# Optimization experiments

Measured on AMD Instinct MI355X. Metric: run time of the kernel, lower is better.

## Reference

```python
import jax, jax.numpy as jnp
import numpy as np

B, T, D = 2, 1024, 1024
H = 8            # num_heads
DK = 128         # head_k_dim
DV = 128         # head_v_dim
M = 128          # num_slots (== head_k_dim by default)
K = 32           # topk
EPS = 1e-5
SCALE = 1.0


def _rmsnorm(x, w, eps=EPS):
    return x * jax.lax.rsqrt(jnp.mean(x * x, axis=-1, keepdims=True) + eps) * w


def setup_inputs() -> dict:
    key = jax.random.key(0)
    ks = jax.random.split(key, 12)
    def lin(k, fan_in, fan_out):
        return jax.random.normal(k, (fan_in, fan_out), jnp.float32) / np.sqrt(fan_in).astype(np.float32)
    hidden_states = jax.random.normal(ks[0], (B, T, D), jnp.float32)
    Wq = lin(ks[1], D, H * DK)
    Wk = lin(ks[2], D, H * DK)
    Wv = lin(ks[3], D, H * DV)
    Wr = lin(ks[4], D, H * M)
    Wa = lin(ks[5], D, H)
    # Mamba2-style decay params
    A_log = jnp.log(jax.random.uniform(ks[6], (H,), jnp.float32, 1e-3, 16.0))
    dt = jnp.exp(jax.random.uniform(ks[7], (H,), jnp.float32) * (np.log(0.1) - np.log(0.001)) + np.log(0.001))
    dt = jnp.clip(dt, 1e-4, None)
    dt_bias = dt + jnp.log(-jnp.expm1(-dt))
    q_norm_w = jnp.ones((DK,), jnp.float32) + 0.01 * jax.random.normal(ks[8], (DK,), jnp.float32)
    k_norm_w = jnp.ones((DK,), jnp.float32) + 0.01 * jax.random.normal(ks[9], (DK,), jnp.float32)
    g_norm_w = jnp.ones((D,), jnp.float32) + 0.01 * jax.random.normal(ks[10], (D,), jnp.float32)
    Wo = lin(ks[11], H * DV, D)
    return dict(hidden_states=hidden_states, Wq=Wq, Wk=Wk, Wv=Wv, Wr=Wr, Wa=Wa,
                A_log=A_log, dt_bias=dt_bias, q_norm_w=q_norm_w, k_norm_w=k_norm_w,
                g_norm_w=g_norm_w, Wo=Wo)


def reference(hidden_states, Wq, Wk, Wv, Wr, Wa, A_log, dt_bias, q_norm_w, k_norm_w, g_norm_w, Wo):
    b, t, d = hidden_states.shape
    # projections
    q = (hidden_states @ Wq).reshape(b, t, H, DK)
    k = (hidden_states @ Wk).reshape(b, t, H, DK)
    v = jax.nn.silu((hidden_states @ Wv).reshape(b, t, H, DV))
    router = (hidden_states @ Wr).reshape(b, t, H, M)
    # Mamba2 decay (log-space, per head)
    f_head = -jnp.exp(A_log) * jax.nn.softplus(hidden_states @ Wa + dt_bias)  # [b,t,H]
    # swish feature map + per-head RMSNorm
    q = _rmsnorm(jax.nn.silu(q), q_norm_w)
    k = _rmsnorm(jax.nn.silu(k), k_norm_w)
    # sigmoid router scores, top-k slot routing (eval: no gumbel noise)
    scores = jax.nn.sigmoid(router)                    # [b,t,H,M]
    top_w, top_i = jax.lax.top_k(scores, K)            # [b,t,H,K]
    top_w = top_w / (jnp.sum(top_w, axis=-1, keepdims=True) + 1e-9)
    n = b * t * H
    rows = jnp.arange(n)[:, None]
    s_multihot = jnp.zeros((n, M), scores.dtype).at[rows, top_i.reshape(n, K)].set(
        top_w.reshape(n, K)).reshape(b, t, H, M)
    f = f_head[..., None] * s_multihot                 # [b,t,H,M], log decay per slot
    s = 1.0 - jnp.exp(f)                               # write gate per slot
    # decayed linear-attention recurrence over slots (M == DK):
    #   S_t[i,j] = exp(f_t[i]) * S_{t-1}[i,j] + s_t[i]*k_t[i]*v_t[j]
    #   o_t[j]   = scale * sum_i q_t[i] * S_t[i,j]
    def step(S, xs):
        q_t, k_t, v_t, f_t, s_t = xs                   # [b,H,*]
        S = jnp.exp(f_t)[..., None] * S + (s_t * k_t)[..., None] * v_t[..., None, :]
        o_t = jnp.einsum('bhk,bhkv->bhv', q_t, S) * SCALE
        return S, o_t
    xs = tuple(jnp.swapaxes(a, 0, 1) for a in (q, k, v, f, s))  # time-major
    S0 = jnp.zeros((b, H, DK, DV), q.dtype)
    _, o = jax.lax.scan(step, S0, xs)                  # o: [t,b,H,DV]
    o = jnp.swapaxes(o, 0, 1).reshape(b, t, H * DV)
    o = _rmsnorm(o, g_norm_w)                          # g_norm over hidden_size
    return o @ Wo
```

## Files before the change

### kernel.cpp

```cpp
#include <hip/hip_runtime.h>
#include <stdint.h>
#include <stddef.h>

#define H_ 8
#define T_ 1024

typedef __attribute__((ext_vector_type(8))) short s16x8;
typedef __attribute__((ext_vector_type(4))) float f32x4;
typedef __attribute__((ext_vector_type(16))) float f32x16;

static __device__ __forceinline__ unsigned short f2bf(float f){
  unsigned u = __float_as_uint(f);
  u += 0x7fffu + ((u >> 16) & 1u);
  return (unsigned short)(u >> 16);
}
static __device__ __forceinline__ float bf2f(unsigned short b){
  return __uint_as_float(((unsigned)b) << 16);
}
static __device__ __forceinline__ unsigned int pack_hl(float x){
  unsigned short h = f2bf(x);
  unsigned short l = f2bf(x - bf2f(h));
  return ((unsigned int)h << 16) | l;
}
static __device__ __forceinline__ void gl_lds16(const unsigned short* g, unsigned short* l){
  __builtin_amdgcn_global_load_lds((const __attribute__((address_space(1))) unsigned int*)g,
                                   (__attribute__((address_space(3))) unsigned int*)l,
                                   16, 0, 0);
}

__global__ void prep_k(const float* __restrict__ X, const float* __restrict__ Wa,
                       const float* __restrict__ A_log, const float* __restrict__ dtb,
                       unsigned short* __restrict__ hi, unsigned short* __restrict__ lo,
                       float* __restrict__ fh){
  __shared__ float xs[1024];
  int n = blockIdx.x, tid = threadIdx.x;
  size_t base = (size_t)n*1024 + tid*4;
  float4 x = *(const float4*)&X[base];
  *(float4*)&xs[tid*4] = x;
  float v[4] = {x.x,x.y,x.z,x.w};
  ushort4 h4, l4;
  unsigned short hh[4], ll[4];
#pragma unroll
  for(int j=0;j<4;j++){ hh[j]=f2bf(v[j]); ll[j]=f2bf(v[j]-bf2f(hh[j])); }
  h4.x=hh[0];h4.y=hh[1];h4.z=hh[2];h4.w=hh[3];
  l4.x=ll[0];l4.y=ll[1];l4.z=ll[2];l4.w=ll[3];
  *(ushort4*)&hi[base] = h4;
  *(ushort4*)&lo[base] = l4;
  __syncthreads();
  int h = tid>>5, l = tid&31;
  float s = 0.f;
  for(int k=l;k<1024;k+=32) s += xs[k]*Wa[(size_t)k*8 + h];
  s += __shfl_xor(s,1); s += __shfl_xor(s,2); s += __shfl_xor(s,4);
  s += __shfl_xor(s,8); s += __shfl_xor(s,16);
  if(l==0){
    float z = s + dtb[h];
    float sp = (z > 20.f) ? z : log1pf(expf(z));
    fh[(size_t)n*8 + h] = -expf(A_log[h]) * sp;
  }
}

__global__ void wtrans(const float* __restrict__ Wq, const float* __restrict__ Wk,
                       const float* __restrict__ Wv, const float* __restrict__ Wr,
                       const float* __restrict__ Wo,
                       unsigned short* __restrict__ WcatT3, unsigned short* __restrict__ WrThi,
                       unsigned short* __restrict__ WrTlo, unsigned short* __restrict__ WoT){
  __shared__ float tile[32][33];
  int z = blockIdx.z;
  const float* src = (z==0)?Wq:(z==1)?Wk:(z==2)?Wv:(z==3)?Wr:Wo;
  int c0 = blockIdx.x*32;
  int k0 = blockIdx.y*32;
  int tx = threadIdx.x, ty = threadIdx.y;
#pragma unroll
  for(int r=0;r<32;r+=8)
    tile[ty+r][tx] = src[(size_t)(k0+ty+r)*1024 + c0 + tx];
  __syncthreads();
#pragma unroll
  for(int r=0;r<32;r+=8){
    int c = c0 + ty + r;
    int k = k0 + tx;
    float v = tile[tx][ty+r];
    if(z < 3){
      WcatT3[((size_t)(z*1024 + c))*1024 + k] = f2bf(v);
    } else if(z == 3){
      unsigned short hv = f2bf(v);
      WrThi[(size_t)c*1024 + k] = hv;
      WrTlo[(size_t)c*1024 + k] = f2bf(v - bf2f(hv));
    } else {
      WoT[(size_t)c*1024 + k] = f2bf(v);
    }
  }
}

__launch_bounds__(256)
__global__ void gemm_fused(const unsigned short* __restrict__ Xhi, const unsigned short* __restrict__ Xlo,
                           const unsigned short* __restrict__ WcatT3, const unsigned short* __restrict__ WrThi,
                           const unsigned short* __restrict__ WrTlo,
                           float* __restrict__ C1, float* __restrict__ Rp){
  __shared__ unsigned short As[128*32];
  __shared__ unsigned short Bs[128*32];
  int bid = blockIdx.x;
  int blk = (bid&7)*96 + (bid>>3);
  const unsigned short *Ap, *Bp;
  float* Cout;
  int bx, by, N;
  if(blk < 384){
    bx = blk%24; by = blk/24; N = 3072;
    Ap = Xhi; Bp = WcatT3; Cout = C1;
  } else {
    int rb = blk-384;
    int seg = rb>>7, t = rb&127;
    bx = t&7; by = t>>3; N = 1024;
    Ap = (seg==2) ? Xlo : Xhi;
    Bp = (seg==1) ? WrTlo : WrThi;
    Cout = Rp + (size_t)seg*2048*1024;
  }
  int tid = threadIdx.x;
  int mBase = by*128, nBase = bx*128;
  int w = tid>>6, lane = tid&63, wr = w>>1, wc = w&1;
  int kg = lane>>4, l15 = lane&15;
  f32x4 acc[4][4];
#pragma unroll
  for(int i=0;i<4;i++)
#pragma unroll
    for(int j=0;j<4;j++) acc[i][j] = (f32x4){0.f,0.f,0.f,0.f};
  int srow = tid>>2, scc = (tid&3) ^ ((srow>>1)&3);
  const unsigned short* gA = Ap + (size_t)(mBase + srow)*1024 + scc*8;
  const unsigned short* gB = Bp + (size_t)(nBase + srow)*1024 + scc*8;
  for(int kb=0; kb<1024; kb+=32){
    gl_lds16(gA + kb,                    &As[tid*8]);
    gl_lds16(gA + (size_t)64*1024 + kb,  &As[2048 + tid*8]);
    gl_lds16(gB + kb,                    &Bs[tid*8]);
    gl_lds16(gB + (size_t)64*1024 + kb,  &Bs[2048 + tid*8]);
    __syncthreads();
    s16x8 afr[4], bfr[4];
#pragma unroll
    for(int f=0;f<4;f++){
      int r = f*16 + l15;
      int xr = (kg ^ ((r>>1)&3))*8;
      afr[f] = *(const s16x8*)&As[(wr*64 + r)*32 + xr];
      bfr[f] = *(const s16x8*)&Bs[(wc*64 + r)*32 + xr];
    }
#pragma unroll
    for(int fm=0;fm<4;fm++)
#pragma unroll
      for(int fn=0;fn<4;fn++)
        acc[fm][fn] = __builtin_amdgcn_mfma_f32_16x16x32_bf16(afr[fm], bfr[fn], acc[fm][fn], 0,0,0);
    __syncthreads();
  }
#pragma unroll
  for(int fm=0;fm<4;fm++)
#pragma unroll
    for(int fn=0;fn<4;fn++){
      int col = nBase + wc*64 + fn*16 + l15;
      int row = mBase + wr*64 + fm*16 + kg*4;
#pragma unroll
      for(int r=0;r<4;r++) Cout[(size_t)(row+r)*N + col] = acc[fm][fn][r];
    }
}

__launch_bounds__(256)
__global__ void gemm_out(const unsigned short* __restrict__ A,
                         const unsigned short* __restrict__ BT,
                         float* __restrict__ C){
  __shared__ unsigned short As[128*32];
  __shared__ unsigned short Bs[64*32];
  const int K = 1024, N = 1024;
  int tid = threadIdx.x;
  int mBase = blockIdx.y*128, nBase = blockIdx.x*64;
  int w = tid>>6, lane = tid&63;
  int mh = w>>1, nh = w&1;
  int kg = lane>>4, l15 = lane&15;
  f32x4 acc[4][2];
#pragma unroll
  for(int i=0;i<4;i++)
#pragma unroll
    for(int j=0;j<2;j++) acc[i][j] = (f32x4){0.f,0.f,0.f,0.f};
  int srow = tid>>2, scc = (tid&3) ^ ((srow>>1)&3);
  const unsigned short* gA = A  + (size_t)(mBase + srow)*K + scc*8;
  const unsigned short* gB = BT + (size_t)(nBase + srow)*K + scc*8;
  for(int kb=0; kb<K; kb+=32){
    gl_lds16(gA + kb,              &As[tid*8]);
    gl_lds16(gA + (size_t)64*K + kb, &As[2048 + tid*8]);
    gl_lds16(gB + kb,              &Bs[tid*8]);
    __syncthreads();
    s16x8 afr[4], bfr[2];
#pragma unroll
    for(int f=0;f<4;f++){
      int r = f*16 + l15;
      afr[f] = *(const s16x8*)&As[(mh*64 + r)*32 + (kg ^ ((r>>1)&3))*8];
    }
#pragma unroll
    for(int f=0;f<2;f++){
      int r = f*16 + l15;
      bfr[f] = *(const s16x8*)&Bs[(nh*32 + r)*32 + (kg ^ ((r>>1)&3))*8];
    }
#pragma unroll
    for(int fm=0;fm<4;fm++)
#pragma unroll
      for(int fn=0;fn<2;fn++)
        acc[fm][fn] = __builtin_amdgcn_mfma_f32_16x16x32_bf16(afr[fm], bfr[fn], acc[fm][fn], 0,0,0);
    __syncthreads();
  }
#pragma unroll
  for(int fm=0;fm<4;fm++)
#pragma unroll
    for(int fn=0;fn<2;fn++){
      int col = nBase + nh*32 + fn*16 + l15;
      int row = mBase + mh*64 + fm*16 + kg*4;
#pragma unroll
      for(int r=0;r<4;r++) C[(size_t)(row+r)*N + col] = acc[fm][fn][r];
    }
}

__launch_bounds__(128)
__global__ void postproc(const float* __restrict__ C1, const float* __restrict__ Rp,
                         const float* __restrict__ fh, const float* __restrict__ qw,
                         const float* __restrict__ kw,
                         float* __restrict__ Qd, float* __restrict__ Wt,
                         float* __restrict__ Fd, float* __restrict__ Vd){
  __shared__ unsigned long long keys[128];
  __shared__ float red[2];
  int blk = blockIdx.x;
  int n = blk>>3, h = blk&7;
  int i = threadIdx.x;
  int b = n>>10, t = n&1023;
  size_t base = ((size_t)(b*H_ + h)*T_ + t)*128 + i;
  size_t cb = (size_t)n*3072;
  size_t rb = (size_t)n*1024 + h*128 + i;
  float qraw = C1[cb + h*128 + i];
  float kraw = C1[cb + 1024 + h*128 + i];
  float vraw = C1[cb + 2048 + h*128 + i];
  float rlog = Rp[rb] + Rp[2048ull*1024 + rb] + Rp[2ull*2048*1024 + rb];
  float qs = qraw/(1.f+expf(-qraw));
  float ks = kraw/(1.f+expf(-kraw));
  float vv = vraw/(1.f+expf(-vraw));
  float si = 1.f/(1.f+expf(-rlog));
  unsigned long long ki = (((unsigned long long)__float_as_uint(si)) << 7) | (unsigned)(127 - i);
  keys[i] = ki;
  __syncthreads();
  int cnt = 0;
#pragma unroll 8
  for(int j=0;j<128;j+=2){
    ulonglong2 k2 = *(const ulonglong2*)&keys[j];
    cnt += (k2.x > ki);
    cnt += (k2.y > ki);
  }
  bool sel = cnt < 32;
  float x;
  x = qs*qs;
  x+=__shfl_xor(x,1);x+=__shfl_xor(x,2);x+=__shfl_xor(x,4);x+=__shfl_xor(x,8);x+=__shfl_xor(x,16);x+=__shfl_xor(x,32);
  __syncthreads(); if((i&63)==0) red[i>>6]=x; __syncthreads();
  float qn = qs * rsqrtf((red[0]+red[1])/128.f + 1e-5f) * qw[i];
  x = ks*ks;
  x+=__shfl_xor(x,1);x+=__shfl_xor(x,2);x+=__shfl_xor(x,4);x+=__shfl_xor(x,8);x+=__shfl_xor(x,16);x+=__shfl_xor(x,32);
  __syncthreads(); if((i&63)==0) red[i>>6]=x; __syncthreads();
  float kn = ks * rsqrtf((red[0]+red[1])/128.f + 1e-5f) * kw[i];
  x = sel ? si : 0.f;
  x+=__shfl_xor(x,1);x+=__shfl_xor(x,2);x+=__shfl_xor(x,4);x+=__shfl_xor(x,8);x+=__shfl_xor(x,16);x+=__shfl_xor(x,32);
  __syncthreads(); if((i&63)==0) red[i>>6]=x; __syncthreads();
  float wsum = red[0]+red[1];
  float wgt = sel ? si/(wsum + 1e-9f) : 0.f;
  float f = fh[(size_t)n*8 + h] * wgt;
  Qd[base] = qn;
  Wt[base] = (1.f - expf(f)) * kn;
  Fd[base] = f;
  Vd[base] = vv;
}

__launch_bounds__(256)
__global__ void chunk_sum(float* __restrict__ Fd, const float* __restrict__ Wt,
                          const float* __restrict__ Vd, float* __restrict__ dS,
                          float* __restrict__ E){
  __shared__ float Fc[32][132];
  __shared__ float Kh[32][132];
  int blk = blockIdx.x, bh = blk>>5, c = blk&31;
  int tid = threadIdx.x;
  int w = tid>>6, lane = tid&63;
  size_t fbase = ((size_t)bh*T_ + (size_t)c*32)*128;
#pragma unroll
  for(int v=0; v<4; v++){
    int e = v*1024 + tid*4;
    int t2 = e>>7, i0 = e&127;
    float4 f4 = *(const float4*)&Fd[fbase + e];
    *(float4*)&Fc[t2][i0] = f4;
  }
  __syncthreads();
  if(tid < 128){
    float a = 0.f;
    for(int t2=0;t2<32;t2++){ a += Fc[t2][tid]; Fc[t2][tid] = a; }
  }
  __syncthreads();
#pragma unroll
  for(int v=0; v<4; v++){
    int e = v*1024 + tid*4;
    int t2 = e>>7, i0 = e&127;
    float4 fc4 = *(const float4*)&Fc[t2][i0];
    *(float4*)&Fd[fbase + e] = fc4;
    float4 ft  = *(const float4*)&Fc[31][i0];
    float4 w4  = *(const float4*)&Wt[fbase + e];
    float4 kh;
    kh.x = w4.x * expf(ft.x - fc4.x);
    kh.y = w4.y * expf(ft.y - fc4.y);
    kh.z = w4.z * expf(ft.z - fc4.z);
    kh.w = w4.w * expf(ft.w - fc4.w);
    *(float4*)&Kh[t2][i0] = kh;
  }
  if(tid < 128) E[((size_t)bh*32 + c)*128 + tid] = expf(Fc[31][tid]);
  __syncthreads();
  int ig = lane>>3, jg = lane&7;
  const float* Vp = Vd + fbase;
  f32x4 acc[4][4];
#pragma unroll
  for(int a=0;a<4;a++)
#pragma unroll
    for(int q=0;q<4;q++) acc[a][q] = (f32x4){0.f,0.f,0.f,0.f};
#pragma unroll 4
  for(int t2=0;t2<32;t2++){
    float4 kq = *(const float4*)&Kh[t2][w*32 + ig*4];
    float4 v0 = *(const float4*)&Vp[t2*128 + jg*4];
    float4 v1 = *(const float4*)&Vp[t2*128 + jg*4 + 32];
    float4 v2 = *(const float4*)&Vp[t2*128 + jg*4 + 64];
    float4 v3 = *(const float4*)&Vp[t2*128 + jg*4 + 96];
    float kk[4] = {kq.x,kq.y,kq.z,kq.w};
#pragma unroll
    for(int a=0;a<4;a++){
      acc[a][0] += kk[a]*(f32x4){v0.x,v0.y,v0.z,v0.w};
      acc[a][1] += kk[a]*(f32x4){v1.x,v1.y,v1.z,v1.w};
      acc[a][2] += kk[a]*(f32x4){v2.x,v2.y,v2.z,v2.w};
      acc[a][3] += kk[a]*(f32x4){v3.x,v3.y,v3.z,v3.w};
    }
  }
  size_t dbase = (size_t)blk*16384;
#pragma unroll
  for(int q=0;q<4;q++)
#pragma unroll
    for(int jj=0;jj<4;jj++){
      float4 o4 = make_float4(acc[0][q][jj],acc[1][q][jj],acc[2][q][jj],acc[3][q][jj]);
      *(float4*)&dS[dbase + (size_t)(jg*4 + 32*q + jj)*128 + w*32 + ig*4] = o4;
    }
}

__global__ void scan_k(float* __restrict__ dS, const float* __restrict__ E){
  int g = blockIdx.x*256 + threadIdx.x;
  int bh = g>>14, e = g&16383;
  int i = e&127;
  float S = 0.f;
  for(int c=0;c<32;c++){
    size_t off = ((size_t)(bh*32 + c))*16384 + e;
    float d  = dS[off];
    float Ec = E[((size_t)(bh*32 + c))*128 + i];
    dS[off] = S;
    S = Ec*S + d;
  }
}

__launch_bounds__(256)
__global__ void chunk_out(const float* __restrict__ Qd, const float* __restrict__ Wt,
                          const float* __restrict__ Fd, const float* __restrict__ Vd,
                          const float* __restrict__ ST, float* __restrict__ O){
  __shared__ unsigned int qtP[32][132];
  __shared__ unsigned int ktP[32][132];
  __shared__ unsigned int Vt[128][36];
  __shared__ float Amat[32][40];
  int blk = blockIdx.x, bh = blk>>5, c = blk&31;
  int b = bh>>3, h = bh&7;
  int tid = threadIdx.x, w = tid>>6, lane = tid&63;
  int m = lane&31, hi = lane>>5;
  size_t fbase = ((size_t)bh*T_ + (size_t)c*32)*128;
#pragma unroll
  for(int p=0;p<4;p++){
    int e = p*1024 + tid*4;
    int t2 = e>>7, i0 = e&127;
    float4 f4 = *(const float4*)&Fd[fbase + e];
    float4 q4 = *(const float4*)&Qd[fbase + e];
    float4 w4 = *(const float4*)&Wt[fbase + e];
    float fv[4] = {f4.x,f4.y,f4.z,f4.w};
    float qv[4] = {q4.x,q4.y,q4.z,q4.w};
    float wv[4] = {w4.x,w4.y,w4.z,w4.w};
    uint4 qp, kp;
    unsigned int qa[4], ka[4];
#pragma unroll
    for(int j=0;j<4;j++){
      float ef = expf(fv[j]);
      qa[j] = pack_hl(qv[j]*ef);
      ka[j] = pack_hl(wv[j]/ef);
    }
    qp.x=qa[0]; qp.y=qa[1]; qp.z=qa[2]; qp.w=qa[3];
    kp.x=ka[0]; kp.y=ka[1]; kp.z=ka[2]; kp.w=ka[3];
    *(uint4*)&qtP[t2][i0] = qp;
    *(uint4*)&ktP[t2][i0] = kp;
  }
  {
    int n = tid&127, th = (tid>>7)*16;
    unsigned int vp[16];
#pragma unroll
    for(int j=0;j<16;j++) vp[j] = pack_hl(Vd[fbase + (size_t)(th+j)*128 + n]);
#pragma unroll
    for(int j=0;j<16;j+=4){
      uint4 v4; v4.x=vp[j]; v4.y=vp[j+1]; v4.z=vp[j+2]; v4.w=vp[j+3];
      *(uint4*)&Vt[n][th+j] = v4;
    }
  }
  __syncthreads();
  if(w == 0){
    f32x16 am;
#pragma unroll
    for(int r=0;r<16;r++) am[r] = 0.f;
#pragma unroll
    for(int s=0;s<8;s++){
      int ko = s*16 + hi*8;
      uint4 qa = *(const uint4*)&qtP[m][ko];
      uint4 qb = *(const uint4*)&qtP[m][ko+4];
      uint4 ka = *(const uint4*)&ktP[m][ko];
      uint4 kb = *(const uint4*)&ktP[m][ko+4];
      s16x8 qh, ql, kh, kl;
      unsigned int qw_[8] = {qa.x,qa.y,qa.z,qa.w,qb.x,qb.y,qb.z,qb.w};
      unsigned int kw_[8] = {ka.x,ka.y,ka.z,ka.w,kb.x,kb.y,kb.z,kb.w};
#pragma unroll
      for(int j=0;j<8;j++){
        qh[j]=(short)(qw_[j]>>16); ql[j]=(short)(qw_[j]&0xffff);
        kh[j]=(short)(kw_[j]>>16); kl[j]=(short)(kw_[j]&0xffff);
      }
      am = __builtin_amdgcn_mfma_f32_32x32x16_bf16(qh, kh, am, 0,0,0);
      am = __builtin_amdgcn_mfma_f32_32x32x16_bf16(qh, kl, am, 0,0,0);
      am = __builtin_amdgcn_mfma_f32_32x32x16_bf16(ql, kh, am, 0,0,0);
    }
#pragma unroll
    for(int r=0;r<16;r++){
      int rm = (r&3) + 8*(r>>2) + 4*hi;
      Amat[rm][m] = (m <= rm) ? am[r] : 0.f;
    }
  }
  f32x16 oacc;
#pragma unroll
  for(int r=0;r<16;r++) oacc[r] = 0.f;
  const float* Sp = ST + (size_t)blk*16384 + (size_t)(w*32 + m)*128;
#pragma unroll
  for(int s=0;s<8;s++){
    int ko = s*16 + hi*8;
    uint4 qa = *(const uint4*)&qtP[m][ko];
    uint4 qb = *(const uint4*)&qtP[m][ko+4];
    s16x8 qh, ql;
    unsigned int qw_[8] = {qa.x,qa.y,qa.z,qa.w,qb.x,qb.y,qb.z,qb.w};
#pragma unroll
    for(int j=0;j<8;j++){ qh[j]=(short)(qw_[j]>>16); ql[j]=(short)(qw_[j]&0xffff); }
    float4 s0 = *(const float4*)&Sp[ko];
    float4 s1 = *(const float4*)&Sp[ko+4];
    float sv[8] = {s0.x,s0.y,s0.z,s0.w,s1.x,s1.y,s1.z,s1.w};
    s16x8 sh, sl;
#pragma unroll
    for(int j=0;j<8;j++){
      unsigned short hh = f2bf(sv[j]);
      sh[j] = (short)hh; sl[j] = (short)f2bf(sv[j]-bf2f(hh));
    }
    oacc = __builtin_amdgcn_mfma_f32_32x32x16_bf16(qh, sh, oacc, 0,0,0);
    oacc = __builtin_amdgcn_mfma_f32_32x32x16_bf16(qh, sl, oacc, 0,0,0);
    oacc = __builtin_amdgcn_mfma_f32_32x32x16_bf16(ql, sh, oacc, 0,0,0);
  }
  __syncthreads();
#pragma unroll
  for(int s=0;s<2;s++){
    int uo = s*16 + hi*8;
    float4 a0 = *(const float4*)&Amat[m][uo];
    float4 a1 = *(const float4*)&Amat[m][uo+4];
    float av[8] = {a0.x,a0.y,a0.z,a0.w,a1.x,a1.y,a1.z,a1.w};
    s16x8 ah, al;
#pragma unroll
    for(int j=0;j<8;j++){
      unsigned short hh = f2bf(av[j]);
      ah[j] = (short)hh; al[j] = (short)f2bf(av[j]-bf2f(hh));
    }
    uint4 v0 = *(const uint4*)&Vt[w*32 + m][uo];
    uint4 v1 = *(const uint4*)&Vt[w*32 + m][uo+4];
    unsigned int vw[8] = {v0.x,v0.y,v0.z,v0.w,v1.x,v1.y,v1.z,v1.w};
    s16x8 vh, vl;
#pragma unroll
    for(int j=0;j<8;j++){ vh[j]=(short)(vw[j]>>16); vl[j]=(short)(vw[j]&0xffff); }
    oacc = __builtin_amdgcn_mfma_f32_32x32x16_bf16(ah, vh, oacc, 0,0,0);
    oacc = __builtin_amdgcn_mfma_f32_32x32x16_bf16(ah, vl, oacc, 0,0,0);
    oacc = __builtin_amdgcn_mfma_f32_32x32x16_bf16(al, vh, oacc, 0,0,0);
  }
#pragma unroll
  for(int r=0;r<16;r++){
    int tok = (r&3) + 8*(r>>2) + 4*hi;
    O[((size_t)(b*T_ + c*32 + tok))*1024 + h*128 + w*32 + m] = oacc[r];
  }
}

__global__ void gnorm_k(const float* __restrict__ Ob, const float* __restrict__ gw,
                        unsigned short* __restrict__ On){
  __shared__ float red[4];
  int n = blockIdx.x, tid = threadIdx.x;
  size_t base = (size_t)n*1024 + tid*4;
  float4 x = *(const float4*)&Ob[base];
  float ss = x.x*x.x + x.y*x.y + x.z*x.z + x.w*x.w;
  ss+=__shfl_xor(ss,1);ss+=__shfl_xor(ss,2);ss+=__shfl_xor(ss,4);
  ss+=__shfl_xor(ss,8);ss+=__shfl_xor(ss,16);ss+=__shfl_xor(ss,32);
  if((tid&63)==0) red[tid>>6]=ss;
  __syncthreads();
  float sc = rsqrtf((red[0]+red[1]+red[2]+red[3])/1024.f + 1e-5f);
  float4 g = *(const float4*)&gw[tid*4];
  ushort4 o4;
  o4.x=f2bf(x.x*sc*g.x); o4.y=f2bf(x.y*sc*g.y);
  o4.z=f2bf(x.z*sc*g.z); o4.w=f2bf(x.w*sc*g.w);
  *(ushort4*)&On[base]=o4;
}

extern "C" void kernel_launch(void* const* d_in, const int* in_sizes, int n_in,
                              void* d_out, int out_size, void* d_ws, size_t ws_size,
                              hipStream_t stream){
  const float* hs   = (const float*)d_in[0];
  const float* Wq   = (const float*)d_in[1];
  const float* Wk   = (const float*)d_in[2];
  const float* Wv   = (const float*)d_in[3];
  const float* Wr   = (const float*)d_in[4];
  const float* Wa   = (const float*)d_in[5];
  const float* A_log= (const float*)d_in[6];
  const float* dtb  = (const float*)d_in[7];
  const float* qw   = (const float*)d_in[8];
  const float* kw   = (const float*)d_in[9];
  const float* gw   = (const float*)d_in[10];
  const float* Wo   = (const float*)d_in[11];
  float* out = (float*)d_out;

  char* wsp = (char*)d_ws;
  size_t off = 0;
  auto alloc = [&](size_t bytes)->void*{ void* p = wsp + off; off += (bytes + 255) & ~(size_t)255; return p; };
  unsigned short* Xhi    = (unsigned short*)alloc(2048ull*1024*2);
  unsigned short* Xlo    = (unsigned short*)alloc(2048ull*1024*2);
  unsigned short* WcatT3 = (unsigned short*)alloc(3072ull*1024*2);
  unsigned short* WrThi  = (unsigned short*)alloc(1024ull*1024*2);
  unsigned short* WrTlo  = (unsigned short*)alloc(1024ull*1024*2);
  unsigned short* WoT    = (unsigned short*)alloc(1024ull*1024*2);
  float* C1 = (float*)alloc(2048ull*3072*4);
  float* fh = (float*)alloc(2048ull*8*4);
  float* Qd = (float*)alloc(16ull*1024*128*4);
  float* Wt = (float*)alloc(16ull*1024*128*4);
  float* Fd = (float*)alloc(16ull*1024*128*4);
  float* Vd = (float*)alloc(16ull*1024*128*4);
  float* E  = (float*)alloc(16ull*32*128*4);
  float* dS = (float*)alloc(16ull*32*16384*4);
  float* Ob = (float*)alloc(2048ull*1024*4);
  unsigned short* On = (unsigned short*)alloc(2048ull*1024*2);
  float* Rp = dS;
  (void)ws_size; (void)in_sizes; (void)n_in; (void)out_size;

  prep_k     <<<dim3(2048),        dim3(256),   0, stream>>>(hs, Wa, A_log, dtb, Xhi, Xlo, fh);
  wtrans     <<<dim3(32,32,5),     dim3(32,8),  0, stream>>>(Wq,Wk,Wv,Wr,Wo, WcatT3,WrThi,WrTlo,WoT);
  gemm_fused <<<dim3(768),         dim3(256),   0, stream>>>(Xhi, Xlo, WcatT3, WrThi, WrTlo, C1, Rp);
  postproc   <<<dim3(16384),       dim3(128),   0, stream>>>(C1, Rp, fh, qw, kw, Qd, Wt, Fd, Vd);
  chunk_sum  <<<dim3(512),         dim3(256),   0, stream>>>(Fd, Wt, Vd, dS, E);
  scan_k     <<<dim3(1024),        dim3(256),   0, stream>>>(dS, E);
  chunk_out  <<<dim3(512),         dim3(256),   0, stream>>>(Qd, Wt, Fd, Vd, dS, Ob);
  gnorm_k    <<<dim3(2048),        dim3(256),   0, stream>>>(Ob, gw, On);
  gemm_out   <<<dim3(16,16),       dim3(256),   0, stream>>>(On, WoT, out);
}
```

Before: 264.2 us.

## Deepen GEMM K-tiles to 64, vectorize postproc per token and scan with float4

Both GEMM kernels now stage 64-wide K tiles with an 8-way XOR swizzle, which halves the number of barrier-separated iterations and does two MFMA sub-steps per tile. Postproc now handles all 8 heads of a token in one 256-thread block, with 4 elements per thread, float4 loads and stores, and wave-level reductions in place of shared-memory reductions. The scan kernel processes 4 state elements per thread with float4 accesses. The trade-off is double the LDS per GEMM block, which may lower occupancy, and more registers per thread in postproc.

```diff
diff --git a/kernel.cpp b/kernel.cpp
--- a/kernel.cpp
+++ b/kernel.cpp
@@ -96,8 +96,8 @@
                            const unsigned short* __restrict__ WcatT3, const unsigned short* __restrict__ WrThi,
                            const unsigned short* __restrict__ WrTlo,
                            float* __restrict__ C1, float* __restrict__ Rp){
-  __shared__ unsigned short As[128*32];
-  __shared__ unsigned short Bs[128*32];
+  __shared__ unsigned short As[128*64];
+  __shared__ unsigned short Bs[128*64];
   int bid = blockIdx.x;
   int blk = (bid&7)*96 + (bid>>3);
   const unsigned short *Ap, *Bp;
@@ -108,8 +108,8 @@
     Ap = Xhi; Bp = WcatT3; Cout = C1;
   } else {
     int rb = blk-384;
-    int seg = rb>>7, t = rb&127;
-    bx = t&7; by = t>>3; N = 1024;
+    int seg = rb>>7, t2 = rb&127;
+    bx = t2&7; by = t2>>3; N = 1024;
     Ap = (seg==2) ? Xlo : Xhi;
     Bp = (seg==1) ? WrTlo : WrThi;
     Cout = Rp + (size_t)seg*2048*1024;
@@ -123,28 +123,39 @@
   for(int i=0;i<4;i++)
 #pragma unroll
     for(int j=0;j<4;j++) acc[i][j] = (f32x4){0.f,0.f,0.f,0.f};
-  int srow = tid>>2, scc = (tid&3) ^ ((srow>>1)&3);
-  const unsigned short* gA = Ap + (size_t)(mBase + srow)*1024 + scc*8;
-  const unsigned short* gB = Bp + (size_t)(nBase + srow)*1024 + scc*8;
-  for(int kb=0; kb<1024; kb+=32){
-    gl_lds16(gA + kb,                    &As[tid*8]);
-    gl_lds16(gA + (size_t)64*1024 + kb,  &As[2048 + tid*8]);
-    gl_lds16(gB + kb,                    &Bs[tid*8]);
-    gl_lds16(gB + (size_t)64*1024 + kb,  &Bs[2048 + tid*8]);
+  size_t aoff[4], boff[4];
+#pragma unroll
+  for(int p=0;p<4;p++){
+    int c = p*256 + tid;
+    int row = c>>3, sc = c&7, c8 = sc ^ (row&7);
+    aoff[p] = (size_t)(mBase+row)*1024 + c8*8;
+    boff[p] = (size_t)(nBase+row)*1024 + c8*8;
+  }
+  for(int kb=0; kb<1024; kb+=64){
+#pragma unroll
+    for(int p=0;p<4;p++){
+      gl_lds16(Ap + aoff[p] + kb, &As[(p*256+tid)*8]);
+      gl_lds16(Bp + boff[p] + kb, &Bs[(p*256+tid)*8]);
+    }
     __syncthreads();
-    s16x8 afr[4], bfr[4];
-#pragma unroll
-    for(int f=0;f<4;f++){
-      int r = f*16 + l15;
-      int xr = (kg ^ ((r>>1)&3))*8;
-      afr[f] = *(const s16x8*)&As[(wr*64 + r)*32 + xr];
-      bfr[f] = *(const s16x8*)&Bs[(wc*64 + r)*32 + xr];
-    }
-#pragma unroll
-    for(int fm=0;fm<4;fm++)
-#pragma unroll
-      for(int fn=0;fn<4;fn++)
-        acc[fm][fn] = __builtin_amdgcn_mfma_f32_16x16x32_bf16(afr[fm], bfr[fn], acc[fm][fn], 0,0,0);
+#pragma unroll
+    for(int kk=0;kk<2;kk++){
+      s16x8 afr[4], bfr[4];
+#pragma unroll
+      for(int f=0;f<4;f++){
+        int rA = wr*64 + f*16 + l15;
+        int rB = wc*64 + f*16 + l15;
+        int cA = (kk*4 + kg) ^ (rA&7);
+        int cB = (kk*4 + kg) ^ (rB&7);
+        afr[f] = *(const s16x8*)&As[rA*64 + cA*8];
+        bfr[f] = *(const s16x8*)&Bs[rB*64 + cB*8];
+      }
+#pragma unroll
+      for(int fm=0;fm<4;fm++)
+#pragma unroll
+        for(int fn=0;fn<4;fn++)
+          acc[fm][fn] = __builtin_amdgcn_mfma_f32_16x16x32_bf16(afr[fm], bfr[fn], acc[fm][fn], 0,0,0);
+    }
     __syncthreads();
   }
 #pragma unroll
@@ -162,8 +173,8 @@
 __global__ void gemm_out(const unsigned short* __restrict__ A,
                          const unsigned short* __restrict__ BT,
                          float* __restrict__ C){
-  __shared__ unsigned short As[128*32];
-  __shared__ unsigned short Bs[64*32];
+  __shared__ unsigned short As[128*64];
+  __shared__ unsigned short Bs[64*64];
   const int K = 1024, N = 1024;
   int tid = threadIdx.x;
   int mBase = blockIdx.y*128, nBase = blockIdx.x*64;
@@ -175,30 +186,44 @@
   for(int i=0;i<4;i++)
 #pragma unroll
     for(int j=0;j<2;j++) acc[i][j] = (f32x4){0.f,0.f,0.f,0.f};
-  int srow = tid>>2, scc = (tid&3) ^ ((srow>>1)&3);
-  const unsigned short* gA = A  + (size_t)(mBase + srow)*K + scc*8;
-  const unsigned short* gB = BT + (size_t)(nBase + srow)*K + scc*8;
-  for(int kb=0; kb<K; kb+=32){
-    gl_lds16(gA + kb,              &As[tid*8]);
-    gl_lds16(gA + (size_t)64*K + kb, &As[2048 + tid*8]);
-    gl_lds16(gB + kb,              &Bs[tid*8]);
+  size_t aoff[4], boff[2];
+#pragma unroll
+  for(int p=0;p<4;p++){
+    int c = p*256 + tid;
+    int row = c>>3, sc = c&7, c8 = sc ^ (row&7);
+    aoff[p] = (size_t)(mBase+row)*K + c8*8;
+  }
+#pragma unroll
+  for(int p=0;p<2;p++){
+    int c = p*256 + tid;
+    int row = c>>3, sc = c&7, c8 = sc ^ (row&7);
+    boff[p] = (size_t)(nBase+row)*K + c8*8;
+  }
+  for(int kb=0; kb<K; kb+=64){
+#pragma unroll
+    for(int p=0;p<4;p++) gl_lds16(A + aoff[p] + kb, &As[(p*256+tid)*8]);
+#pragma unroll
+    for(int p=0;p<2;p++) gl_lds16(BT + boff[p] + kb, &Bs[(p*256+tid)*8]);
     __syncthreads();
-    s16x8 afr[4], bfr[2];
-#pragma unroll
-    for(int f=0;f<4;f++){
-      int r = f*16 + l15;
-      afr[f] = *(const s16x8*)&As[(mh*64 + r)*32 + (kg ^ ((r>>1)&3))*8];
-    }
-#pragma unroll
-    for(int f=0;f<2;f++){
-      int r = f*16 + l15;
-      bfr[f] = *(const s16x8*)&Bs[(nh*32 + r)*32 + (kg ^ ((r>>1)&3))*8];
-    }
-#pragma unroll
-    for(int fm=0;fm<4;fm++)
-#pragma unroll
-      for(int fn=0;fn<2;fn++)
-        acc[fm][fn] = __builtin_amdgcn_mfma_f32_16x16x32_bf16(afr[fm], bfr[fn], acc[fm][fn], 0,0,0);
+#pragma unroll
+    for(int kk=0;kk<2;kk++){
+      s16x8 afr[4], bfr[2];
+#pragma unroll
+      for(int f=0;f<4;f++){
+        int r = mh*64 + f*16 + l15;
+        afr[f] = *(const s16x8*)&As[r*64 + ((kk*4+kg) ^ (r&7))*8];
+      }
+#pragma unroll
+      for(int f=0;f<2;f++){
+        int r = nh*32 + f*16 + l15;
+        bfr[f] = *(const s16x8*)&Bs[r*64 + ((kk*4+kg) ^ (r&7))*8];
+      }
+#pragma unroll
+      for(int fm=0;fm<4;fm++)
+#pragma unroll
+        for(int fn=0;fn<2;fn++)
+          acc[fm][fn] = __builtin_amdgcn_mfma_f32_16x16x32_bf16(afr[fm], bfr[fn], acc[fm][fn], 0,0,0);
+    }
     __syncthreads();
   }
 #pragma unroll
@@ -212,59 +237,85 @@
     }
 }
 
-__launch_bounds__(128)
+__launch_bounds__(256)
 __global__ void postproc(const float* __restrict__ C1, const float* __restrict__ Rp,
                          const float* __restrict__ fh, const float* __restrict__ qw,
                          const float* __restrict__ kw,
                          float* __restrict__ Qd, float* __restrict__ Wt,
                          float* __restrict__ Fd, float* __restrict__ Vd){
-  __shared__ unsigned long long keys[128];
-  __shared__ float red[2];
-  int blk = blockIdx.x;
-  int n = blk>>3, h = blk&7;
-  int i = threadIdx.x;
-  int b = n>>10, t = n&1023;
-  size_t base = ((size_t)(b*H_ + h)*T_ + t)*128 + i;
+  __shared__ unsigned long long keys[8][128];
+  int n = blockIdx.x;
+  int t = threadIdx.x;
+  int b = n>>10, tt = n&1023;
+  int h = t>>5;
+  int i0 = (t&31)*4;
   size_t cb = (size_t)n*3072;
-  size_t rb = (size_t)n*1024 + h*128 + i;
-  float qraw = C1[cb + h*128 + i];
-  float kraw = C1[cb + 1024 + h*128 + i];
-  float vraw = C1[cb + 2048 + h*128 + i];
-  float rlog = Rp[rb] + Rp[2048ull*1024 + rb] + Rp[2ull*2048*1024 + rb];
-  float qs = qraw/(1.f+expf(-qraw));
-  float ks = kraw/(1.f+expf(-kraw));
-  float vv = vraw/(1.f+expf(-vraw));
-  float si = 1.f/(1.f+expf(-rlog));
-  unsigned long long ki = (((unsigned long long)__float_as_uint(si)) << 7) | (unsigned)(127 - i);
-  keys[i] = ki;
-  __syncthreads();
-  int cnt = 0;
-#pragma unroll 8
+  size_t rbase = (size_t)n*1024 + h*128 + i0;
+  float4 q4 = *(const float4*)&C1[cb + h*128 + i0];
+  float4 k4 = *(const float4*)&C1[cb + 1024 + h*128 + i0];
+  float4 v4 = *(const float4*)&C1[cb + 2048 + h*128 + i0];
+  float4 r0 = *(const float4*)&Rp[rbase];
+  float4 r1 = *(const float4*)&Rp[2048ull*1024 + rbase];
+  float4 r2 = *(const float4*)&Rp[2ull*2048*1024 + rbase];
+  float qv[4] = {q4.x,q4.y,q4.z,q4.w};
+  float kv[4] = {k4.x,k4.y,k4.z,k4.w};
+  float vv4[4] = {v4.x,v4.y,v4.z,v4.w};
+  float rl[4] = {r0.x+r1.x+r2.x, r0.y+r1.y+r2.y, r0.z+r1.z+r2.z, r0.w+r1.w+r2.w};
+  float qs[4], ks[4], vv[4], si[4];
+  unsigned long long ki[4];
+#pragma unroll
+  for(int j=0;j<4;j++){
+    qs[j] = qv[j]/(1.f+expf(-qv[j]));
+    ks[j] = kv[j]/(1.f+expf(-kv[j]));
+    vv[j] = vv4[j]/(1.f+expf(-vv4[j]));
+    si[j] = 1.f/(1.f+expf(-rl[j]));
+    ki[j] = (((unsigned long long)__float_as_uint(si[j])) << 7) | (unsigned)(127 - (i0+j));
+    keys[h][i0+j] = ki[j];
+  }
+  __syncthreads();
+  int cnt[4] = {0,0,0,0};
+#pragma unroll 4
   for(int j=0;j<128;j+=2){
-    ulonglong2 k2 = *(const ulonglong2*)&keys[j];
-    cnt += (k2.x > ki);
-    cnt += (k2.y > ki);
-  }
-  bool sel = cnt < 32;
+    ulonglong2 k2 = *(const ulonglong2*)&keys[h][j];
+#pragma unroll
+    for(int m=0;m<4;m++){
+      cnt[m] += (k2.x > ki[m]);
+      cnt[m] += (k2.y > ki[m]);
+    }
+  }
+  bool sel[4];
+#pragma unroll
+  for(int m=0;m<4;m++) sel[m] = cnt[m] < 32;
   float x;
-  x = qs*qs;
-  x+=__shfl_xor(x,1);x+=__shfl_xor(x,2);x+=__shfl_xor(x,4);x+=__shfl_xor(x,8);x+=__shfl_xor(x,16);x+=__shfl_xor(x,32);
-  __syncthreads(); if((i&63)==0) red[i>>6]=x; __syncthreads();
-  float qn = qs * rsqrtf((red[0]+red[1])/128.f + 1e-5f) * qw[i];
-  x = ks*ks;
-  x+=__shfl_xor(x,1);x+=__shfl_xor(x,2);x+=__shfl_xor(x,4);x+=__shfl_xor(x,8);x+=__shfl_xor(x,16);x+=__shfl_xor(x,32);
-  __syncthreads(); if((i&63)==0) red[i>>6]=x; __syncthreads();
-  float kn = ks * rsqrtf((red[0]+red[1])/128.f + 1e-5f) * kw[i];
-  x = sel ? si : 0.f;
-  x+=__shfl_xor(x,1);x+=__shfl_xor(x,2);x+=__shfl_xor(x,4);x+=__shfl_xor(x,8);x+=__shfl_xor(x,16);x+=__shfl_xor(x,32);
-  __syncthreads(); if((i&63)==0) red[i>>6]=x; __syncthreads();
-  float wsum = red[0]+red[1];
-  float wgt = sel ? si/(wsum + 1e-9f) : 0.f;
-  float f = fh[(size_t)n*8 + h] * wgt;
-  Qd[base] = qn;
-  Wt[base] = (1.f - expf(f)) * kn;
-  Fd[base] = f;
-  Vd[base] = vv;
+  x = qs[0]*qs[0]+qs[1]*qs[1]+qs[2]*qs[2]+qs[3]*qs[3];
+  x+=__shfl_xor(x,1);x+=__shfl_xor(x,2);x+=__shfl_xor(x,4);x+=__shfl_xor(x,8);x+=__shfl_xor(x,16);
+  float qrms = rsqrtf(x/128.f + 1e-5f);
+  x = ks[0]*ks[0]+ks[1]*ks[1]+ks[2]*ks[2]+ks[3]*ks[3];
+  x+=__shfl_xor(x,1);x+=__shfl_xor(x,2);x+=__shfl_xor(x,4);x+=__shfl_xor(x,8);x+=__shfl_xor(x,16);
+  float krms = rsqrtf(x/128.f + 1e-5f);
+  x = (sel[0]?si[0]:0.f)+(sel[1]?si[1]:0.f)+(sel[2]?si[2]:0.f)+(sel[3]?si[3]:0.f);
+  x+=__shfl_xor(x,1);x+=__shfl_xor(x,2);x+=__shfl_xor(x,4);x+=__shfl_xor(x,8);x+=__shfl_xor(x,16);
+  float winv = 1.f/(x + 1e-9f);
+  float fhv = fh[(size_t)n*8 + h];
+  size_t base = ((size_t)((b*H_ + h)*T_) + tt)*128 + i0;
+  float4 qo, wo, fo, vo;
+  float qd[4], wd[4], fd[4];
+#pragma unroll
+  for(int j=0;j<4;j++){
+    float wgt = sel[j] ? si[j]*winv : 0.f;
+    float f = fhv * wgt;
+    qd[j] = qs[j]*qrms*qw[i0+j];
+    wd[j] = (1.f - expf(f)) * (ks[j]*krms*kw[i0+j]);
+    fd[j] = f;
+  }
+  qo.x=qd[0];qo.y=qd[1];qo.z=qd[2];qo.w=qd[3];
+  wo.x=wd[0];wo.y=wd[1];wo.z=wd[2];wo.w=wd[3];
+  fo.x=fd[0];fo.y=fd[1];fo.z=fd[2];fo.w=fd[3];
+  vo.x=vv[0];vo.y=vv[1];vo.z=vv[2];vo.w=vv[3];
+  *(float4*)&Qd[base] = qo;
+  *(float4*)&Wt[base] = wo;
+  *(float4*)&Fd[base] = fo;
+  *(float4*)&Vd[base] = vo;
 }
 
 __launch_bounds__(256)
@@ -342,15 +393,19 @@
 
 __global__ void scan_k(float* __restrict__ dS, const float* __restrict__ E){
   int g = blockIdx.x*256 + threadIdx.x;
-  int bh = g>>14, e = g&16383;
-  int i = e&127;
-  float S = 0.f;
+  int bh = g>>12;
+  int e4 = (g&4095)*4;
+  int i0 = e4 & 127;
+  float4 S = make_float4(0.f,0.f,0.f,0.f);
   for(int c=0;c<32;c++){
-    size_t off = ((size_t)(bh*32 + c))*16384 + e;
-    float d  = dS[off];
-    float Ec = E[((size_t)(bh*32 + c))*128 + i];
-    dS[off] = S;
-    S = Ec*S + d;
+    size_t off = ((size_t)(bh*32 + c))*16384 + e4;
+    float4 d   = *(const float4*)&dS[off];
+    float4 Ec  = *(const float4*)&E[((size_t)(bh*32 + c))*128 + i0];
+    *(float4*)&dS[off] = S;
+    S.x = Ec.x*S.x + d.x;
+    S.y = Ec.y*S.y + d.y;
+    S.z = Ec.z*S.z + d.z;
+    S.w = Ec.w*S.w + d.w;
   }
 }
 
@@ -548,9 +603,9 @@
   prep_k     <<<dim3(2048),        dim3(256),   0, stream>>>(hs, Wa, A_log, dtb, Xhi, Xlo, fh);
   wtrans     <<<dim3(32,32,5),     dim3(32,8),  0, stream>>>(Wq,Wk,Wv,Wr,Wo, WcatT3,WrThi,WrTlo,WoT);
   gemm_fused <<<dim3(768),         dim3(256),   0, stream>>>(Xhi, Xlo, WcatT3, WrThi, WrTlo, C1, Rp);
-  postproc   <<<dim3(16384),       dim3(128),   0, stream>>>(C1, Rp, fh, qw, kw, Qd, Wt, Fd, Vd);
+  postproc   <<<dim3(2048),        dim3(256),   0, stream>>>(C1, Rp, fh, qw, kw, Qd, Wt, Fd, Vd);
   chunk_sum  <<<dim3(512),         dim3(256),   0, stream>>>(Fd, Wt, Vd, dS, E);
-  scan_k     <<<dim3(1024),        dim3(256),   0, stream>>>(dS, E);
+  scan_k     <<<dim3(256),         dim3(256),   0, stream>>>(dS, E);
   chunk_out  <<<dim3(512),         dim3(256),   0, stream>>>(Qd, Wt, Fd, Vd, dS, Ob);
   gnorm_k    <<<dim3(2048),        dim3(256),   0, stream>>>(Ob, gw, On);
   gemm_out   <<<dim3(16,16),       dim3(256),   0, stream>>>(On, WoT, out);
```

Measured after the change: 254.0 us. -3.9%, faster.
